# Optimization experiments

Measured on AMD Instinct MI355X. Metric: run time of the kernel, lower is better.

The kernel has to match this reference:

```python
import jax, jax.numpy as jnp
import numpy as np

D_IN = 1024
D_OUT = 1024
NUM_HEADS = 16
HEAD_DIM = D_OUT // NUM_HEADS


def setup_inputs() -> dict:
    key = jax.random.key(0)
    ks = jax.random.split(key, 6)
    scale = 0.02
    x = jax.random.normal(ks[0], (8, 1024, D_IN), dtype=jnp.float32)
    # weights stored as [in, out] (transposed vs torch Linear.weight)
    W_query = jax.random.normal(ks[1], (D_IN, D_OUT), dtype=jnp.float32) * scale
    W_key = jax.random.normal(ks[2], (D_IN, HEAD_DIM), dtype=jnp.float32) * scale
    W_value = jax.random.normal(ks[3], (D_IN, HEAD_DIM), dtype=jnp.float32) * scale
    W_out = jax.random.normal(ks[4], (D_OUT, D_OUT), dtype=jnp.float32) * scale
    b_out = jax.random.normal(ks[5], (D_OUT,), dtype=jnp.float32) * scale
    return {"x": x, "W_query": W_query, "W_key": W_key, "W_value": W_value,
            "W_out": W_out, "b_out": b_out}


def reference(x, W_query, W_key, W_value, W_out, b_out):
    B, S, _ = x.shape
    H, Dh = NUM_HEADS, HEAD_DIM
    q = (x @ W_query).reshape(B, S, H, Dh).transpose(0, 2, 1, 3)  # [B,H,S,Dh]
    k = x @ W_key      # [B,S,Dh] single shared head
    v = x @ W_value    # [B,S,Dh]
    # scores: broadcast shared K across all query heads (no explicit repeat)
    scores = jnp.einsum("bhqd,bkd->bhqk", q, k)  # [B,H,S,S]
    causal = jnp.triu(jnp.ones((S, S), dtype=bool), k=1)
    scores = jnp.where(causal[None, None], -jnp.inf, scores)
    attn = jax.nn.softmax(scores / np.sqrt(Dh).astype(np.float32), axis=-1)
    # dropout p=0.0 -> identity
    ctx = jnp.einsum("bhqk,bkd->bhqd", attn, v)  # [B,H,S,Dh]
    ctx = ctx.transpose(0, 2, 1, 3).reshape(B, S, H * Dh)
    return ctx @ W_out + b_out
```

## Files before the change

### kernel.cpp

```cpp
#include <hip/hip_runtime.h>

typedef unsigned short u16;
typedef __attribute__((ext_vector_type(8))) short short8;
typedef __attribute__((ext_vector_type(4))) float f32x4;
typedef __attribute__((ext_vector_type(16))) float f32x16;
typedef __attribute__((ext_vector_type(4))) unsigned short u16x4;
typedef __attribute__((ext_vector_type(4))) int i32x4;

__device__ __forceinline__ u16 f2b(float f) {
  unsigned u = __float_as_uint(f);
  unsigned r = (u + 0x7fffu + ((u >> 16) & 1u)) >> 16;
  return (u16)r;
}

__device__ __forceinline__ void gload16(const u16* g, u16* l) {
  __builtin_amdgcn_global_load_lds((const __attribute__((address_space(1))) void*)g,
                                   (__attribute__((address_space(3))) void*)l, 16, 0, 0);
}

__global__ void cvt_bf16(const float* __restrict__ in, u16* __restrict__ out, int n) {
  int i = (blockIdx.x * blockDim.x + threadIdx.x) * 4;
  if (i >= n) return;
  f32x4 v = *(const f32x4*)(in + i);
  u16x4 o;
  o[0] = f2b(v[0]); o[1] = f2b(v[1]); o[2] = f2b(v[2]); o[3] = f2b(v[3]);
  *(u16x4*)(out + i) = o;
}

__global__ void transpose_cvt(const float* __restrict__ in, u16* __restrict__ out, int R, int C) {
  __shared__ float t[32][33];
  int c0 = blockIdx.x * 32, r0 = blockIdx.y * 32;
  int tx = threadIdx.x & 31, ty = threadIdx.x >> 5;
#pragma unroll
  for (int i = 0; i < 32; i += 8)
    t[ty + i][tx] = in[(size_t)(r0 + ty + i) * C + c0 + tx];
  __syncthreads();
#pragma unroll
  for (int i = 0; i < 32; i += 8)
    out[(size_t)(c0 + ty + i) * R + r0 + tx] = f2b(t[tx][ty + i]);
}

#define GEMM_CORE(A_PTR, B_PTR)                                                        \
  __shared__ u16 As[4096];                                                \
  __shared__ u16 Bs[8192];                                               \
  const int tid = threadIdx.x;                                                         \
  const int lane = tid & 63, wid = tid >> 6;                              \
  const int lg = lane >> 4, li = lane & 15;                                            \
  const int wr = wid >> 1, wc = wid & 1;                                               \
  f32x4 acc[2][4] = {};                                                                \
  const int lrow = lane >> 3;                                                \
  const int lslot = lane & 7;                                                          \
  const int scol = 8 * (lslot ^ lrow);                    \
  const u16* Ab = (A_PTR) + (size_t)(m0 + wid * 16 + lrow) * 1024 + scol;              \
  const u16* Bb = (B_PTR) + (size_t)(wid * 32 + lrow) * 1024 + scol;                   \
  u16* const dA = As + wid * 1024;                   \
  u16* const dB = Bs + wid * 2048;                                                     \
  for (int t = 0; t < 16; ++t) {                                                       \
    const int k0 = t * 64;                                                             \
    __syncthreads();                                       \
    gload16(Ab + k0,         dA);                                                      \
    gload16(Ab + k0 + 8192,  dA + 512);                                   \
    _Pragma("unroll")                                                                  \
    for (int c = 0; c < 4; ++c)                                                        \
      gload16(Bb + k0 + c * 8192, dB + c * 512);                                       \
    __syncthreads();                                          \
    _Pragma("unroll")                                                                  \
    for (int kki = 0; kki < 2; ++kki) {                                                \
      short8 af[2], bfr[4];                                                            \
      _Pragma("unroll")                                                                \
      for (int mi = 0; mi < 2; ++mi) {                                                 \
        const int r = wr * 32 + mi * 16 + li;                                          \
        af[mi] = *(const short8*)&As[r * 64 + 8 * ((4 * kki + lg) ^ (r & 7))];         \
      }                                                                                \
      _Pragma("unroll")                                                                \
      for (int ni = 0; ni < 4; ++ni) {                                                 \
        const int r = wc * 64 + ni * 16 + li;                                          \
        bfr[ni] = *(const short8*)&Bs[r * 64 + 8 * ((4 * kki + lg) ^ (r & 7))];        \
      }                                                                                \
      _Pragma("unroll")                                                                \
      for (int mi = 0; mi < 2; ++mi)                                                   \
        _Pragma("unroll")                                                              \
        for (int ni = 0; ni < 4; ++ni)                                                 \
          acc[mi][ni] =                                                                \
              __builtin_amdgcn_mfma_f32_16x16x32_bf16(af[mi], bfr[ni], acc[mi][ni],    \
                                                      0, 0, 0);                        \
    }                                                                                  \
  }

__global__ __launch_bounds__(256) void gemm_proj(
    const u16* __restrict__ A, const u16* __restrict__ BtQ, const u16* __restrict__ BtKV,
    u16* __restrict__ Qp, u16* __restrict__ K3, u16* __restrict__ Vt3, float scaleQ) {
  const int m0 = blockIdx.x * 64;
  const int by = blockIdx.y;
  const bool isQ = (by < 8);
  const int n0 = isQ ? by * 128 : 0;
  GEMM_CORE(A, (isQ ? BtQ + (size_t)n0 * 1024 : BtKV))

#pragma unroll
  for (int mi = 0; mi < 2; ++mi) {
#pragma unroll
    for (int ni = 0; ni < 4; ++ni) {
      const int n = n0 + wc * 64 + ni * 16 + li;
#pragma unroll
      for (int i = 0; i < 4; ++i) {
        const int m = m0 + wr * 32 + mi * 16 + lg * 4 + i;
        const float v = acc[mi][ni][i];
        const int bb = m >> 10, ss = m & 1023;
        const int qt = ss >> 5, sl = ss & 31;
        if (isQ) {
          const int h = n >> 6, dd = n & 63;
          const int t = dd >> 4, h2 = (dd >> 3) & 1, j = dd & 7;
          Qp[(((((size_t)bb * 16 + h) * 32 + qt) * 4 + t) * 2 + h2) * 256 + sl * 8 + j] =
              f2b(v * scaleQ);
        } else if (n < 64) {
          const int t = n >> 4, h2 = (n >> 3) & 1, j = n & 7;
          K3[(((((size_t)bb * 32 + qt) * 4 + t) * 2 + h2) * 32 + sl) * 8 + j] = f2b(v);
        } else {
          const int d = n - 64;
          const int ks = sl >> 4, rem = sl & 15;
          const int h2 = (rem >> 2) & 1, j = (rem & 3) | ((rem >> 3) << 2);
          Vt3[(((((size_t)bb * 32 + qt) * 2 + ks) * 2 + h2) * 64 + d) * 8 + j] = f2b(v);
        }
      }
    }
  }
}

__global__ __launch_bounds__(256) void gemm_out(
    const u16* __restrict__ A, const u16* __restrict__ Bt,
    float* __restrict__ Cf, const float* __restrict__ bias) {
  const int m0 = blockIdx.x * 64;
  const int n0 = blockIdx.y * 128;
  GEMM_CORE(A, Bt + (size_t)n0 * 1024)

#pragma unroll
  for (int mi = 0; mi < 2; ++mi)
#pragma unroll
    for (int ni = 0; ni < 4; ++ni) {
      const int n = n0 + wc * 64 + ni * 16 + li;
#pragma unroll
      for (int i = 0; i < 4; ++i) {
        const int m = m0 + wr * 32 + mi * 16 + lg * 4 + i;
        Cf[(size_t)m * 1024 + n] = acc[mi][ni][i] + bias[n];
      }
    }
}

__global__ __launch_bounds__(256, 4) void attn_mqa6(
    const u16* __restrict__ qp, const u16* __restrict__ k3,
    const u16* __restrict__ vt3, u16* __restrict__ paro, float* __restrict__ pl) {
  __shared__ u16 lk[2][2048];
  __shared__ u16 lv[2][2048];
  const int lane = threadIdx.x & 63, wid = threadIdx.x >> 6;
  const int bx = blockIdx.x;
  const int qt = 31 - (bx >> 6);
  const int s  = (bx >> 5) & 1;
  const int g  = bx & 31;
  const int b  = g >> 2;
  const int h  = (g & 3) * 4 + wid;
  const int l31 = lane & 31, hi = lane >> 5;
  const int n0t = (qt + 2) >> 1;
  const int kb_ = s ? n0t : 0;
  const int ke  = s ? qt + 1 : n0t;
  const int task = (b * 16 + h) * 32 + qt;

  const u16* k3b = k3 + (size_t)b * 65536;
  const u16* v3b = vt3 + (size_t)b * 65536;
  const int soff = wid * 512 + lane * 8;

  const u16* qbase = qp + (size_t)task * 2048 + hi * 256 + l31 * 8;
  short8 qa[4];
#pragma unroll
  for (int t = 0; t < 4; ++t) qa[t] = *(const short8*)(qbase + t * 512);

  f32x16 acc0 = {}, acc1 = {};
  float lsum = 0.f;

  if (kb_ < ke) {
    gload16(k3b + (size_t)kb_ * 2048 + soff, &lk[0][wid * 512]);
    gload16(v3b + (size_t)kb_ * 2048 + soff, &lv[0][wid * 512]);
    __syncthreads();

    int par = 0;
    for (int kvt = kb_; kvt < ke; ++kvt, par ^= 1) {
      if (kvt + 1 < ke) {
        gload16(k3b + (size_t)(kvt + 1) * 2048 + soff, &lk[par ^ 1][wid * 512]);
        gload16(v3b + (size_t)(kvt + 1) * 2048 + soff, &lv[par ^ 1][wid * 512]);
      }
      short8 kc[4];
#pragma unroll
      for (int t = 0; t < 4; ++t)
        kc[t] = *(const short8*)&lk[par][l31 * 8 + (t * 2 + hi) * 256];
      const u16* vtt = &lv[par][hi * 512 + l31 * 8];
      const short8 vf0 = *(const short8*)(vtt);
      const short8 vf1 = *(const short8*)(vtt + 1024);
      const short8 vf2 = *(const short8*)(vtt + 256);
      const short8 vf3 = *(const short8*)(vtt + 1280);

      f32x16 st = {};
#pragma unroll
      for (int t = 0; t < 4; ++t)
        st = __builtin_amdgcn_mfma_f32_32x32x16_bf16(kc[t], qa[t], st, 0, 0, 0);

      if (kvt == qt) {
#pragma unroll
        for (int r = 0; r < 16; ++r) {
          const int crow = (r & 3) + 8 * (r >> 2) + 4 * hi;
          if (crow > l31) st[r] = -1e38f;
        }
      }
      float e[16];
#pragma unroll
      for (int r = 0; r < 16; ++r)
        asm("v_exp_f32 %0, %1" : "=v"(e[r]) : "v"(st[r]));
      lsum += ((e[0] + e[1]) + (e[2] + e[3])) + ((e[4] + e[5]) + (e[6] + e[7])) +
              (((e[8] + e[9]) + (e[10] + e[11])) + ((e[12] + e[13]) + (e[14] + e[15])));

      unsigned pw0, pw1, pw2, pw3, pw4, pw5, pw6, pw7;
      asm("v_cvt_pk_bf16_f32 %0, %1, %2" : "=v"(pw0) : "v"(e[0]),  "v"(e[1]));
      asm("v_cvt_pk_bf16_f32 %0, %1, %2" : "=v"(pw1) : "v"(e[2]),  "v"(e[3]));
      asm("v_cvt_pk_bf16_f32 %0, %1, %2" : "=v"(pw2) : "v"(e[4]),  "v"(e[5]));
      asm("v_cvt_pk_bf16_f32 %0, %1, %2" : "=v"(pw3) : "v"(e[6]),  "v"(e[7]));
      asm("v_cvt_pk_bf16_f32 %0, %1, %2" : "=v"(pw4) : "v"(e[8]),  "v"(e[9]));
      asm("v_cvt_pk_bf16_f32 %0, %1, %2" : "=v"(pw5) : "v"(e[10]), "v"(e[11]));
      asm("v_cvt_pk_bf16_f32 %0, %1, %2" : "=v"(pw6) : "v"(e[12]), "v"(e[13]));
      asm("v_cvt_pk_bf16_f32 %0, %1, %2" : "=v"(pw7) : "v"(e[14]), "v"(e[15]));
      i32x4 w0 = {(int)pw0, (int)pw1, (int)pw2, (int)pw3};
      i32x4 w1 = {(int)pw4, (int)pw5, (int)pw6, (int)pw7};
      const short8 pa0 = *(const short8*)&w0;
      const short8 pa1 = *(const short8*)&w1;

      acc0 = __builtin_amdgcn_mfma_f32_32x32x16_bf16(pa0, vf0, acc0, 0, 0, 0);
      acc0 = __builtin_amdgcn_mfma_f32_32x32x16_bf16(pa1, vf1, acc0, 0, 0, 0);
      acc1 = __builtin_amdgcn_mfma_f32_32x32x16_bf16(pa0, vf2, acc1, 0, 0, 0);
      acc1 = __builtin_amdgcn_mfma_f32_32x32x16_bf16(pa1, vf3, acc1, 0, 0, 0);

      __syncthreads();
    }
  }

  const float lfull = lsum + __shfl_xor(lsum, 32, 64);
  u16* pbase = paro + ((size_t)task * 2 + s) * 2048;
#pragma unroll
  for (int r = 0; r < 16; ++r) {
    const int crow = (r & 3) + 8 * (r >> 2) + 4 * hi;
    pbase[crow * 64 + l31] = f2b(acc0[r]);
    pbase[crow * 64 + 32 + l31] = f2b(acc1[r]);
  }
  if (hi == 0) pl[((size_t)task * 2 + s) * 32 + l31] = lfull;
}

__global__ __launch_bounds__(256) void attn_combine(
    const u16* __restrict__ paro, const float* __restrict__ pl, u16* __restrict__ ctxb) {
  const int grp = threadIdx.x >> 6, tid = threadIdx.x & 63;
  const int task = blockIdx.x * 4 + grp;
  const int qt = task & 31, hh = (task >> 5) & 15, bb = task >> 9;
  const unsigned* p0 = (const unsigned*)(paro + (size_t)task * 4096);
  const unsigned* p1 = p0 + 1024;
  const float* lt = pl + (size_t)task * 64;
  const int rh = tid >> 5, cc = tid & 31;
  unsigned* co = (unsigned*)ctxb;
#pragma unroll 4
  for (int it = 0; it < 16; ++it) {
    const int r = it * 2 + rh;
    const float inv = 1.0f / (lt[r] + lt[32 + r]);
    const unsigned a = p0[r * 32 + cc], bu = p1[r * 32 + cc];
    const float v0 = (__uint_as_float(a << 16) + __uint_as_float(bu << 16)) * inv;
    const float v1 = (__uint_as_float(a & 0xffff0000u) + __uint_as_float(bu & 0xffff0000u)) * inv;
    const unsigned pk = (unsigned)f2b(v0) | ((unsigned)f2b(v1) << 16);
    co[(size_t)(bb * 1024 + qt * 32 + r) * 512 + hh * 32 + cc] = pk;
  }
}

extern "C" void kernel_launch(void* const* d_in, const int* in_sizes, int n_in,
                              void* d_out, int out_size, void* d_ws, size_t ws_size,
                              hipStream_t stream) {
  const float* x  = (const float*)d_in[0];
  const float* Wq = (const float*)d_in[1];
  const float* Wk = (const float*)d_in[2];
  const float* Wv = (const float*)d_in[3];
  const float* Wo = (const float*)d_in[4];
  const float* bo = (const float*)d_in[5];
  float* out = (float*)d_out;

  u16* ws16 = (u16*)d_ws;
  const size_t M1 = 1u << 20;
  u16* woT  = ws16;
  u16* qp   = ws16 + 1 * M1;
  u16* k3   = ws16 + 9 * M1;
  u16* vt3  = ws16 + 9 * M1 + (M1 >> 1);
  u16* xb   = ws16 + 10 * M1;
  u16* wqT  = ws16 + 18 * M1;
  u16* wkT  = ws16 + 19 * M1;
  u16* wvT  = wkT + 65536;
  u16* paro = ws16 + 10 * M1;
  float* pl = (float*)(ws16 + 26 * M1);
  u16* ctx  = qp;

  cvt_bf16<<<8192, 256, 0, stream>>>(x, xb, 8192 * 1024);
  transpose_cvt<<<dim3(32, 32), 256, 0, stream>>>(Wq, wqT, 1024, 1024);
  transpose_cvt<<<dim3(2, 32), 256, 0, stream>>>(Wk, wkT, 1024, 64);
  transpose_cvt<<<dim3(2, 32), 256, 0, stream>>>(Wv, wvT, 1024, 64);
  transpose_cvt<<<dim3(32, 32), 256, 0, stream>>>(Wo, woT, 1024, 1024);

  const float SCL = 0.125f * 1.44269504088896340736f;
  gemm_proj<<<dim3(128, 9), 256, 0, stream>>>(xb, wqT, wkT, qp, k3, vt3, SCL);

  attn_mqa6<<<2048, 256, 0, stream>>>(qp, k3, vt3, paro, pl);
  attn_combine<<<1024, 256, 0, stream>>>(paro, pl, ctx);

  gemm_out<<<dim3(128, 8), 256, 0, stream>>>(ctx, woT, out, bo);
}
```

Baseline: 115.4 us.

## Double-buffer GEMM LDS tiles and drop split-KV attention with combine kernel

The shared GEMM core now double-buffers its A and B tiles in LDS, issuing the next k-tile's global-to-LDS loads before computing on the current tile, so load latency overlaps MFMA work. The attention kernel no longer splits each query tile's KV range into two halves. It uses 128-thread blocks, two heads per block, each covering the full causal KV range, and normalises and writes bf16 context directly. This removes the separate combine kernel and its partial-output round trip through memory. The cost is double the LDS in the GEMMs and less parallelism, with more load imbalance across causal tiles in attention.

```diff
diff --git a/kernel.cpp b/kernel.cpp
--- a/kernel.cpp
+++ b/kernel.cpp
@@ -41,41 +41,49 @@
 }
 
 #define GEMM_CORE(A_PTR, B_PTR)                                                        \
-  __shared__ u16 As[4096];                                                \
-  __shared__ u16 Bs[8192];                                               \
+  __shared__ u16 As[2][4096];                                             \
+  __shared__ u16 Bs[2][8192];                                            \
   const int tid = threadIdx.x;                                                         \
   const int lane = tid & 63, wid = tid >> 6;                              \
   const int lg = lane >> 4, li = lane & 15;                                            \
   const int wr = wid >> 1, wc = wid & 1;                                               \
   f32x4 acc[2][4] = {};                                                                \
-  const int lrow = lane >> 3;                                                \
-  const int lslot = lane & 7;                                                          \
+  const int lrow = lane >> 3, lslot = lane & 7;                                        \
   const int scol = 8 * (lslot ^ lrow);                    \
   const u16* Ab = (A_PTR) + (size_t)(m0 + wid * 16 + lrow) * 1024 + scol;              \
   const u16* Bb = (B_PTR) + (size_t)(wid * 32 + lrow) * 1024 + scol;                   \
-  u16* const dA = As + wid * 1024;                   \
-  u16* const dB = Bs + wid * 2048;                                                     \
-  for (int t = 0; t < 16; ++t) {                                                       \
-    const int k0 = t * 64;                                                             \
-    __syncthreads();                                       \
-    gload16(Ab + k0,         dA);                                                      \
-    gload16(Ab + k0 + 8192,  dA + 512);                                   \
-    _Pragma("unroll")                                                                  \
-    for (int c = 0; c < 4; ++c)                                                        \
-      gload16(Bb + k0 + c * 8192, dB + c * 512);                                       \
-    __syncthreads();                                          \
+  const int dAo = wid * 1024, dBo = wid * 2048;            \
+  gload16(Ab, &As[0][dAo]);                                                            \
+  gload16(Ab + 8192, &As[0][dAo + 512]);                                               \
+  { _Pragma("unroll")                                                                  \
+    for (int c_ = 0; c_ < 4; ++c_) gload16(Bb + c_ * 8192, &Bs[0][dBo + c_ * 512]); }  \
+  asm volatile("s_waitcnt vmcnt(0)" ::: "memory");                                     \
+  __builtin_amdgcn_s_barrier();                                                        \
+  __builtin_amdgcn_sched_barrier(0);                                                   \
+  int par = 0;                                                                         \
+  for (int t = 0; t < 16; ++t, par ^= 1) {                                             \
+    if (t < 15) {                                           \
+      const int k1 = (t + 1) * 64;                                                     \
+      gload16(Ab + k1, &As[par ^ 1][dAo]);                                             \
+      gload16(Ab + k1 + 8192, &As[par ^ 1][dAo + 512]);                                \
+      _Pragma("unroll")                                                                \
+      for (int c_ = 0; c_ < 4; ++c_)                                                   \
+        gload16(Bb + k1 + c_ * 8192, &Bs[par ^ 1][dBo + c_ * 512]);                    \
+    }                                                                                  \
+    const u16* Ac = As[par];                                                           \
+    const u16* Bc = Bs[par];                                                           \
     _Pragma("unroll")                                                                  \
     for (int kki = 0; kki < 2; ++kki) {                                                \
       short8 af[2], bfr[4];                                                            \
       _Pragma("unroll")                                                                \
       for (int mi = 0; mi < 2; ++mi) {                                                 \
         const int r = wr * 32 + mi * 16 + li;                                          \
-        af[mi] = *(const short8*)&As[r * 64 + 8 * ((4 * kki + lg) ^ (r & 7))];         \
+        af[mi] = *(const short8*)&Ac[r * 64 + 8 * ((4 * kki + lg) ^ (r & 7))];         \
       }                                                                                \
       _Pragma("unroll")                                                                \
       for (int ni = 0; ni < 4; ++ni) {                                                 \
         const int r = wc * 64 + ni * 16 + li;                                          \
-        bfr[ni] = *(const short8*)&Bs[r * 64 + 8 * ((4 * kki + lg) ^ (r & 7))];        \
+        bfr[ni] = *(const short8*)&Bc[r * 64 + 8 * ((4 * kki + lg) ^ (r & 7))];        \
       }                                                                                \
       _Pragma("unroll")                                                                \
       for (int mi = 0; mi < 2; ++mi)                                                   \
@@ -85,6 +93,9 @@
               __builtin_amdgcn_mfma_f32_16x16x32_bf16(af[mi], bfr[ni], acc[mi][ni],    \
                                                       0, 0, 0);                        \
     }                                                                                  \
+    asm volatile("s_waitcnt vmcnt(0)" ::: "memory");  \
+    __builtin_amdgcn_s_barrier();                     \
+    __builtin_amdgcn_sched_barrier(0);                                                 \
   }
 
 __global__ __launch_bounds__(256) void gemm_proj(
@@ -146,27 +157,26 @@
     }
 }
 
-__global__ __launch_bounds__(256, 4) void attn_mqa6(
+__global__ __launch_bounds__(128, 4) void attn_mqa7(
     const u16* __restrict__ qp, const u16* __restrict__ k3,
-    const u16* __restrict__ vt3, u16* __restrict__ paro, float* __restrict__ pl) {
+    const u16* __restrict__ vt3, u16* __restrict__ ctxb) {
   __shared__ u16 lk[2][2048];
   __shared__ u16 lv[2][2048];
   const int lane = threadIdx.x & 63, wid = threadIdx.x >> 6;
   const int bx = blockIdx.x;
   const int qt = 31 - (bx >> 6);
-  const int s  = (bx >> 5) & 1;
-  const int g  = bx & 31;
-  const int b  = g >> 2;
-  const int h  = (g & 3) * 4 + wid;
+  const int r6 = bx & 63;
+  const int b  = r6 >> 3;
+  const int h  = (r6 & 7) * 2 + wid;
   const int l31 = lane & 31, hi = lane >> 5;
-  const int n0t = (qt + 2) >> 1;
-  const int kb_ = s ? n0t : 0;
-  const int ke  = s ? qt + 1 : n0t;
+  const int q0 = qt * 32;
+  const int ke = qt + 1;
   const int task = (b * 16 + h) * 32 + qt;
 
   const u16* k3b = k3 + (size_t)b * 65536;
   const u16* v3b = vt3 + (size_t)b * 65536;
-  const int soff = wid * 512 + lane * 8;
+  const int soff = wid * 1024 + lane * 8;
+  const int dstw = wid * 1024;
 
   const u16* qbase = qp + (size_t)task * 2048 + hi * 256 + l31 * 8;
   short8 qa[4];
@@ -176,99 +186,81 @@
   f32x16 acc0 = {}, acc1 = {};
   float lsum = 0.f;
 
-  if (kb_ < ke) {
-    gload16(k3b + (size_t)kb_ * 2048 + soff, &lk[0][wid * 512]);
-    gload16(v3b + (size_t)kb_ * 2048 + soff, &lv[0][wid * 512]);
+  gload16(k3b + soff,       &lk[0][dstw]);
+  gload16(k3b + soff + 512, &lk[0][dstw + 512]);
+  gload16(v3b + soff,       &lv[0][dstw]);
+  gload16(v3b + soff + 512, &lv[0][dstw + 512]);
+  __syncthreads();
+
+  int par = 0;
+  for (int kvt = 0; kvt < ke; ++kvt, par ^= 1) {
+    if (kvt + 1 < ke) {
+      const size_t o = (size_t)(kvt + 1) * 2048 + soff;
+      gload16(k3b + o,       &lk[par ^ 1][dstw]);
+      gload16(k3b + o + 512, &lk[par ^ 1][dstw + 512]);
+      gload16(v3b + o,       &lv[par ^ 1][dstw]);
+      gload16(v3b + o + 512, &lv[par ^ 1][dstw + 512]);
+    }
+    short8 kc[4];
+#pragma unroll
+    for (int t = 0; t < 4; ++t)
+      kc[t] = *(const short8*)&lk[par][l31 * 8 + (t * 2 + hi) * 256];
+    const u16* vtt = &lv[par][hi * 512 + l31 * 8];
+    const short8 vf0 = *(const short8*)(vtt);
+    const short8 vf1 = *(const short8*)(vtt + 1024);
+    const short8 vf2 = *(const short8*)(vtt + 256);
+    const short8 vf3 = *(const short8*)(vtt + 1280);
+
+    f32x16 st = {};
+#pragma unroll
+    for (int t = 0; t < 4; ++t)
+      st = __builtin_amdgcn_mfma_f32_32x32x16_bf16(kc[t], qa[t], st, 0, 0, 0);
+
+    if (kvt == qt) {
+#pragma unroll
+      for (int r = 0; r < 16; ++r) {
+        const int crow = (r & 3) + 8 * (r >> 2) + 4 * hi;
+        if (crow > l31) st[r] = -1e38f;
+      }
+    }
+    float e[16];
+#pragma unroll
+    for (int r = 0; r < 16; ++r)
+      asm("v_exp_f32 %0, %1" : "=v"(e[r]) : "v"(st[r]));
+    lsum += ((e[0] + e[1]) + (e[2] + e[3])) + ((e[4] + e[5]) + (e[6] + e[7])) +
+            (((e[8] + e[9]) + (e[10] + e[11])) + ((e[12] + e[13]) + (e[14] + e[15])));
+
+    unsigned pw0, pw1, pw2, pw3, pw4, pw5, pw6, pw7;
+    asm("v_cvt_pk_bf16_f32 %0, %1, %2" : "=v"(pw0) : "v"(e[0]),  "v"(e[1]));
+    asm("v_cvt_pk_bf16_f32 %0, %1, %2" : "=v"(pw1) : "v"(e[2]),  "v"(e[3]));
+    asm("v_cvt_pk_bf16_f32 %0, %1, %2" : "=v"(pw2) : "v"(e[4]),  "v"(e[5]));
+    asm("v_cvt_pk_bf16_f32 %0, %1, %2" : "=v"(pw3) : "v"(e[6]),  "v"(e[7]));
+    asm("v_cvt_pk_bf16_f32 %0, %1, %2" : "=v"(pw4) : "v"(e[8]),  "v"(e[9]));
+    asm("v_cvt_pk_bf16_f32 %0, %1, %2" : "=v"(pw5) : "v"(e[10]), "v"(e[11]));
+    asm("v_cvt_pk_bf16_f32 %0, %1, %2" : "=v"(pw6) : "v"(e[12]), "v"(e[13]));
+    asm("v_cvt_pk_bf16_f32 %0, %1, %2" : "=v"(pw7) : "v"(e[14]), "v"(e[15]));
+    i32x4 w0 = {(int)pw0, (int)pw1, (int)pw2, (int)pw3};
+    i32x4 w1 = {(int)pw4, (int)pw5, (int)pw6, (int)pw7};
+    const short8 pa0 = *(const short8*)&w0;
+    const short8 pa1 = *(const short8*)&w1;
+
+    acc0 = __builtin_amdgcn_mfma_f32_32x32x16_bf16(pa0, vf0, acc0, 0, 0, 0);
+    acc0 = __builtin_amdgcn_mfma_f32_32x32x16_bf16(pa1, vf1, acc0, 0, 0, 0);
+    acc1 = __builtin_amdgcn_mfma_f32_32x32x16_bf16(pa0, vf2, acc1, 0, 0, 0);
+    acc1 = __builtin_amdgcn_mfma_f32_32x32x16_bf16(pa1, vf3, acc1, 0, 0, 0);
+
     __syncthreads();
-
-    int par = 0;
-    for (int kvt = kb_; kvt < ke; ++kvt, par ^= 1) {
-      if (kvt + 1 < ke) {
-        gload16(k3b + (size_t)(kvt + 1) * 2048 + soff, &lk[par ^ 1][wid * 512]);
-        gload16(v3b + (size_t)(kvt + 1) * 2048 + soff, &lv[par ^ 1][wid * 512]);
-      }
-      short8 kc[4];
-#pragma unroll
-      for (int t = 0; t < 4; ++t)
-        kc[t] = *(const short8*)&lk[par][l31 * 8 + (t * 2 + hi) * 256];
-      const u16* vtt = &lv[par][hi * 512 + l31 * 8];
-      const short8 vf0 = *(const short8*)(vtt);
-      const short8 vf1 = *(const short8*)(vtt + 1024);
-      const short8 vf2 = *(const short8*)(vtt + 256);
-      const short8 vf3 = *(const short8*)(vtt + 1280);
-
-      f32x16 st = {};
-#pragma unroll
-      for (int t = 0; t < 4; ++t)
-        st = __builtin_amdgcn_mfma_f32_32x32x16_bf16(kc[t], qa[t], st, 0, 0, 0);
-
-      if (kvt == qt) {
-#pragma unroll
-        for (int r = 0; r < 16; ++r) {
-          const int crow = (r & 3) + 8 * (r >> 2) + 4 * hi;
-          if (crow > l31) st[r] = -1e38f;
-        }
-      }
-      float e[16];
-#pragma unroll
-      for (int r = 0; r < 16; ++r)
-        asm("v_exp_f32 %0, %1" : "=v"(e[r]) : "v"(st[r]));
-      lsum += ((e[0] + e[1]) + (e[2] + e[3])) + ((e[4] + e[5]) + (e[6] + e[7])) +
-              (((e[8] + e[9]) + (e[10] + e[11])) + ((e[12] + e[13]) + (e[14] + e[15])));
-
-      unsigned pw0, pw1, pw2, pw3, pw4, pw5, pw6, pw7;
-      asm("v_cvt_pk_bf16_f32 %0, %1, %2" : "=v"(pw0) : "v"(e[0]),  "v"(e[1]));
-      asm("v_cvt_pk_bf16_f32 %0, %1, %2" : "=v"(pw1) : "v"(e[2]),  "v"(e[3]));
-      asm("v_cvt_pk_bf16_f32 %0, %1, %2" : "=v"(pw2) : "v"(e[4]),  "v"(e[5]));
-      asm("v_cvt_pk_bf16_f32 %0, %1, %2" : "=v"(pw3) : "v"(e[6]),  "v"(e[7]));
-      asm("v_cvt_pk_bf16_f32 %0, %1, %2" : "=v"(pw4) : "v"(e[8]),  "v"(e[9]));
-      asm("v_cvt_pk_bf16_f32 %0, %1, %2" : "=v"(pw5) : "v"(e[10]), "v"(e[11]));
-      asm("v_cvt_pk_bf16_f32 %0, %1, %2" : "=v"(pw6) : "v"(e[12]), "v"(e[13]));
-      asm("v_cvt_pk_bf16_f32 %0, %1, %2" : "=v"(pw7) : "v"(e[14]), "v"(e[15]));
-      i32x4 w0 = {(int)pw0, (int)pw1, (int)pw2, (int)pw3};
-      i32x4 w1 = {(int)pw4, (int)pw5, (int)pw6, (int)pw7};
-      const short8 pa0 = *(const short8*)&w0;
-      const short8 pa1 = *(const short8*)&w1;
-
-      acc0 = __builtin_amdgcn_mfma_f32_32x32x16_bf16(pa0, vf0, acc0, 0, 0, 0);
-      acc0 = __builtin_amdgcn_mfma_f32_32x32x16_bf16(pa1, vf1, acc0, 0, 0, 0);
-      acc1 = __builtin_amdgcn_mfma_f32_32x32x16_bf16(pa0, vf2, acc1, 0, 0, 0);
-      acc1 = __builtin_amdgcn_mfma_f32_32x32x16_bf16(pa1, vf3, acc1, 0, 0, 0);
-
-      __syncthreads();
-    }
   }
 
   const float lfull = lsum + __shfl_xor(lsum, 32, 64);
-  u16* pbase = paro + ((size_t)task * 2 + s) * 2048;
+  const float linv = 1.0f / lfull;
 #pragma unroll
   for (int r = 0; r < 16; ++r) {
     const int crow = (r & 3) + 8 * (r >> 2) + 4 * hi;
-    pbase[crow * 64 + l31] = f2b(acc0[r]);
-    pbase[crow * 64 + 32 + l31] = f2b(acc1[r]);
-  }
-  if (hi == 0) pl[((size_t)task * 2 + s) * 32 + l31] = lfull;
-}
-
-__global__ __launch_bounds__(256) void attn_combine(
-    const u16* __restrict__ paro, const float* __restrict__ pl, u16* __restrict__ ctxb) {
-  const int grp = threadIdx.x >> 6, tid = threadIdx.x & 63;
-  const int task = blockIdx.x * 4 + grp;
-  const int qt = task & 31, hh = (task >> 5) & 15, bb = task >> 9;
-  const unsigned* p0 = (const unsigned*)(paro + (size_t)task * 4096);
-  const unsigned* p1 = p0 + 1024;
-  const float* lt = pl + (size_t)task * 64;
-  const int rh = tid >> 5, cc = tid & 31;
-  unsigned* co = (unsigned*)ctxb;
-#pragma unroll 4
-  for (int it = 0; it < 16; ++it) {
-    const int r = it * 2 + rh;
-    const float inv = 1.0f / (lt[r] + lt[32 + r]);
-    const unsigned a = p0[r * 32 + cc], bu = p1[r * 32 + cc];
-    const float v0 = (__uint_as_float(a << 16) + __uint_as_float(bu << 16)) * inv;
-    const float v1 = (__uint_as_float(a & 0xffff0000u) + __uint_as_float(bu & 0xffff0000u)) * inv;
-    const unsigned pk = (unsigned)f2b(v0) | ((unsigned)f2b(v1) << 16);
-    co[(size_t)(bb * 1024 + qt * 32 + r) * 512 + hh * 32 + cc] = pk;
+    const float lr = __shfl(linv, crow, 64);
+    const size_t mrow = (size_t)(b * 1024 + q0 + crow) * 1024 + h * 64;
+    ctxb[mrow + l31] = f2b(acc0[r] * lr);
+    ctxb[mrow + 32 + l31] = f2b(acc1[r] * lr);
   }
 }
 
@@ -290,12 +282,10 @@
   u16* k3   = ws16 + 9 * M1;
   u16* vt3  = ws16 + 9 * M1 + (M1 >> 1);
   u16* xb   = ws16 + 10 * M1;
+  u16* ctx  = ws16 + 10 * M1;
   u16* wqT  = ws16 + 18 * M1;
   u16* wkT  = ws16 + 19 * M1;
   u16* wvT  = wkT + 65536;
-  u16* paro = ws16 + 10 * M1;
-  float* pl = (float*)(ws16 + 26 * M1);
-  u16* ctx  = qp;
 
   cvt_bf16<<<8192, 256, 0, stream>>>(x, xb, 8192 * 1024);
   transpose_cvt<<<dim3(32, 32), 256, 0, stream>>>(Wq, wqT, 1024, 1024);
@@ -306,8 +296,7 @@
   const float SCL = 0.125f * 1.44269504088896340736f;
   gemm_proj<<<dim3(128, 9), 256, 0, stream>>>(xb, wqT, wkT, qp, k3, vt3, SCL);
 
-  attn_mqa6<<<2048, 256, 0, stream>>>(qp, k3, vt3, paro, pl);
-  attn_combine<<<1024, 256, 0, stream>>>(paro, pl, ctx);
+  attn_mqa7<<<2048, 128, 0, stream>>>(qp, k3, vt3, ctx);
 
   gemm_out<<<dim3(128, 8), 256, 0, stream>>>(ctx, woT, out, bo);
 }
```

New measurement: 125.3 us. 8.6% more time.

## Fuse prep conversion kernels and triple-buffer the output GEMM loads

Applied to the files above, without the earlier changes.

Merges the x bf16 conversion and the four weight transpose-convert launches into a single prep kernel that dispatches on block index, removing four kernel launches. It also adds a triple-buffered GEMM core for the output projection: it prefetches two k-tiles ahead with global_load_lds, waits on vmcnt and uses one barrier per iteration instead of two. This is meant to overlap global loads with MFMA work. The cost is three times the LDS per block, which may reduce occupancy, and the hand-written waitcnt assumes a fixed count of outstanding loads.

```diff
diff --git a/kernel.cpp b/kernel.cpp
--- a/kernel.cpp
+++ b/kernel.cpp
@@ -18,19 +18,30 @@
                                    (__attribute__((address_space(3))) void*)l, 16, 0, 0);
 }
 
-__global__ void cvt_bf16(const float* __restrict__ in, u16* __restrict__ out, int n) {
-  int i = (blockIdx.x * blockDim.x + threadIdx.x) * 4;
-  if (i >= n) return;
-  f32x4 v = *(const f32x4*)(in + i);
-  u16x4 o;
-  o[0] = f2b(v[0]); o[1] = f2b(v[1]); o[2] = f2b(v[2]); o[3] = f2b(v[3]);
-  *(u16x4*)(out + i) = o;
-}
-
-__global__ void transpose_cvt(const float* __restrict__ in, u16* __restrict__ out, int R, int C) {
+__global__ void prep(const float* __restrict__ x, const float* __restrict__ Wq,
+                     const float* __restrict__ Wk, const float* __restrict__ Wv,
+                     const float* __restrict__ Wo, u16* __restrict__ xb,
+                     u16* __restrict__ wqT, u16* __restrict__ wkT,
+                     u16* __restrict__ wvT, u16* __restrict__ woT) {
   __shared__ float t[32][33];
-  int c0 = blockIdx.x * 32, r0 = blockIdx.y * 32;
-  int tx = threadIdx.x & 31, ty = threadIdx.x >> 5;
+  int bid = blockIdx.x;
+  if (bid < 8192) {
+    const int i = (bid * 256 + threadIdx.x) * 4;
+    f32x4 v = *(const f32x4*)(x + i);
+    u16x4 o;
+    o[0] = f2b(v[0]); o[1] = f2b(v[1]); o[2] = f2b(v[2]); o[3] = f2b(v[3]);
+    *(u16x4*)(xb + i) = o;
+    return;
+  }
+  bid -= 8192;
+  const float* in; u16* out; int C, bx, by;
+  if (bid < 1024)      { in = Wq; out = wqT; C = 1024; bx = bid & 31; by = bid >> 5; }
+  else if (bid < 1088) { in = Wk; out = wkT; C = 64;   bid -= 1024; bx = bid & 1; by = bid >> 1; }
+  else if (bid < 1152) { in = Wv; out = wvT; C = 64;   bid -= 1088; bx = bid & 1; by = bid >> 1; }
+  else                 { in = Wo; out = woT; C = 1024; bid -= 1152; bx = bid & 31; by = bid >> 5; }
+  const int R = 1024;
+  const int c0 = bx * 32, r0 = by * 32;
+  const int tx = threadIdx.x & 31, ty = threadIdx.x >> 5;
 #pragma unroll
   for (int i = 0; i < 32; i += 8)
     t[ty + i][tx] = in[(size_t)(r0 + ty + i) * C + c0 + tx];
@@ -48,22 +59,20 @@
   const int lg = lane >> 4, li = lane & 15;                                            \
   const int wr = wid >> 1, wc = wid & 1;                                               \
   f32x4 acc[2][4] = {};                                                                \
-  const int lrow = lane >> 3;                                                \
-  const int lslot = lane & 7;                                                          \
+  const int lrow = lane >> 3, lslot = lane & 7;                                        \
   const int scol = 8 * (lslot ^ lrow);                    \
   const u16* Ab = (A_PTR) + (size_t)(m0 + wid * 16 + lrow) * 1024 + scol;              \
   const u16* Bb = (B_PTR) + (size_t)(wid * 32 + lrow) * 1024 + scol;                   \
-  u16* const dA = As + wid * 1024;                   \
+  u16* const dA = As + wid * 1024;                                                     \
   u16* const dB = Bs + wid * 2048;                                                     \
   for (int t = 0; t < 16; ++t) {                                                       \
     const int k0 = t * 64;                                                             \
-    __syncthreads();                                       \
-    gload16(Ab + k0,         dA);                                                      \
-    gload16(Ab + k0 + 8192,  dA + 512);                                   \
+    __syncthreads();                                                                   \
+    gload16(Ab + k0,        dA);                                                       \
+    gload16(Ab + k0 + 8192, dA + 512);                                                 \
     _Pragma("unroll")                                                                  \
-    for (int c = 0; c < 4; ++c)                                                        \
-      gload16(Bb + k0 + c * 8192, dB + c * 512);                                       \
-    __syncthreads();                                          \
+    for (int c_ = 0; c_ < 4; ++c_) gload16(Bb + k0 + c_ * 8192, dB + c_ * 512);        \
+    __syncthreads();                                                                   \
     _Pragma("unroll")                                                                  \
     for (int kki = 0; kki < 2; ++kki) {                                                \
       short8 af[2], bfr[4];                                                            \
@@ -85,6 +94,67 @@
               __builtin_amdgcn_mfma_f32_16x16x32_bf16(af[mi], bfr[ni], acc[mi][ni],    \
                                                       0, 0, 0);                        \
     }                                                                                  \
+  }
+
+#define GEMM_CORE_DEEP(A_PTR, B_PTR)                                                   \
+  __shared__ u16 As[3][4096];                                                          \
+  __shared__ u16 Bs[3][8192];                                                          \
+  const int tid = threadIdx.x;                                                         \
+  const int lane = tid & 63, wid = tid >> 6;                                           \
+  const int lg = lane >> 4, li = lane & 15;                                            \
+  const int wr = wid >> 1, wc = wid & 1;                                               \
+  f32x4 acc[2][4] = {};                                                                \
+  const int lrow = lane >> 3, lslot = lane & 7;                                        \
+  const int scol = 8 * (lslot ^ lrow);                                                 \
+  const u16* Ab = (A_PTR) + (size_t)(m0 + wid * 16 + lrow) * 1024 + scol;              \
+  const u16* Bb = (B_PTR) + (size_t)(wid * 32 + lrow) * 1024 + scol;                   \
+  const int dAo = wid * 1024, dBo = wid * 2048;                                        \
+  _Pragma("unroll")                                                                    \
+  for (int p = 0; p < 2; ++p) {                                                        \
+    const int kp = p * 64;                                                             \
+    gload16(Ab + kp,        &As[p][dAo]);                                              \
+    gload16(Ab + kp + 8192, &As[p][dAo + 512]);                                        \
+    _Pragma("unroll")                                                                  \
+    for (int c_ = 0; c_ < 4; ++c_) gload16(Bb + kp + c_ * 8192, &Bs[p][dBo + c_ * 512]); \
+  }                                                                                    \
+  int cur = 0;                                                                         \
+  for (int t = 0; t < 16; ++t) {                                                       \
+    if (t < 15) asm volatile("s_waitcnt vmcnt(6)" ::: "memory");                       \
+    else        asm volatile("s_waitcnt vmcnt(0)" ::: "memory");                       \
+    __builtin_amdgcn_s_barrier();                                                      \
+    __builtin_amdgcn_sched_barrier(0);                                                 \
+    if (t + 2 < 16) {                                                                  \
+      const int k2 = (t + 2) * 64;                                                     \
+      const int nb = (cur + 2 >= 3) ? cur - 1 : cur + 2;                               \
+      gload16(Ab + k2,        &As[nb][dAo]);                                           \
+      gload16(Ab + k2 + 8192, &As[nb][dAo + 512]);                                     \
+      _Pragma("unroll")                                                                \
+      for (int c_ = 0; c_ < 4; ++c_) gload16(Bb + k2 + c_ * 8192, &Bs[nb][dBo + c_ * 512]); \
+    }                                                                                  \
+    const u16* Ac = As[cur];                                                           \
+    const u16* Bc = Bs[cur];                                                           \
+    _Pragma("unroll")                                                                  \
+    for (int kki = 0; kki < 2; ++kki) {                                                \
+      short8 af[2], bfr[4];                                                            \
+      _Pragma("unroll")                                                                \
+      for (int mi = 0; mi < 2; ++mi) {                                                 \
+        const int r = wr * 32 + mi * 16 + li;                                          \
+        af[mi] = *(const short8*)&Ac[r * 64 + 8 * ((4 * kki + lg) ^ (r & 7))];         \
+      }                                                                                \
+      _Pragma("unroll")                                                                \
+      for (int ni = 0; ni < 4; ++ni) {                                                 \
+        const int r = wc * 64 + ni * 16 + li;                                          \
+        bfr[ni] = *(const short8*)&Bc[r * 64 + 8 * ((4 * kki + lg) ^ (r & 7))];        \
+      }                                                                                \
+      _Pragma("unroll")                                                                \
+      for (int mi = 0; mi < 2; ++mi)                                                   \
+        _Pragma("unroll")                                                              \
+        for (int ni = 0; ni < 4; ++ni)                                                 \
+          acc[mi][ni] =                                                                \
+              __builtin_amdgcn_mfma_f32_16x16x32_bf16(af[mi], bfr[ni], acc[mi][ni],    \
+                                                      0, 0, 0);                        \
+    }                                                                                  \
+    cur = (cur == 2) ? 0 : cur + 1;                                                    \
   }
 
 __global__ __launch_bounds__(256) void gemm_proj(
@@ -131,7 +201,7 @@
     float* __restrict__ Cf, const float* __restrict__ bias) {
   const int m0 = blockIdx.x * 64;
   const int n0 = blockIdx.y * 128;
-  GEMM_CORE(A, Bt + (size_t)n0 * 1024)
+  GEMM_CORE_DEEP(A, Bt + (size_t)n0 * 1024)
 
 #pragma unroll
   for (int mi = 0; mi < 2; ++mi)
@@ -297,11 +367,7 @@
   float* pl = (float*)(ws16 + 26 * M1);
   u16* ctx  = qp;
 
-  cvt_bf16<<<8192, 256, 0, stream>>>(x, xb, 8192 * 1024);
-  transpose_cvt<<<dim3(32, 32), 256, 0, stream>>>(Wq, wqT, 1024, 1024);
-  transpose_cvt<<<dim3(2, 32), 256, 0, stream>>>(Wk, wkT, 1024, 64);
-  transpose_cvt<<<dim3(2, 32), 256, 0, stream>>>(Wv, wvT, 1024, 64);
-  transpose_cvt<<<dim3(32, 32), 256, 0, stream>>>(Wo, woT, 1024, 1024);
+  prep<<<10368, 256, 0, stream>>>(x, Wq, Wk, Wv, Wo, xb, wqT, wkT, wvT, woT);
 
   const float SCL = 0.125f * 1.44269504088896340736f;
   gemm_proj<<<dim3(128, 9), 256, 0, stream>>>(xb, wqT, wkT, qp, k3, vt3, SCL);
```

Measured after the change: 115.4 us. About the same (+0.1%).

## Fuse split-KV attention combine into attention kernel and merge prep kernels

Applied to the files above, without the earlier changes.

Restructures the attention kernel so each block runs two heads, each split across two waves over KV ranges. The two halves are merged in-block through shared memory, normalised and written directly as bf16 context. This removes the separate combine kernel and the partial-output and row-sum round trip through global memory. The five conversion and transpose launches are also folded into one prep kernel, cutting launch overhead. In exchange, the causal split leaves waves idle on unequal KV ranges, blocks now load different K/V tiles per wave pair, and there is an extra block-wide sync for the merge.

```diff
diff --git a/kernel.cpp b/kernel.cpp
--- a/kernel.cpp
+++ b/kernel.cpp
@@ -18,19 +18,30 @@
                                    (__attribute__((address_space(3))) void*)l, 16, 0, 0);
 }
 
-__global__ void cvt_bf16(const float* __restrict__ in, u16* __restrict__ out, int n) {
-  int i = (blockIdx.x * blockDim.x + threadIdx.x) * 4;
-  if (i >= n) return;
-  f32x4 v = *(const f32x4*)(in + i);
-  u16x4 o;
-  o[0] = f2b(v[0]); o[1] = f2b(v[1]); o[2] = f2b(v[2]); o[3] = f2b(v[3]);
-  *(u16x4*)(out + i) = o;
-}
-
-__global__ void transpose_cvt(const float* __restrict__ in, u16* __restrict__ out, int R, int C) {
+__global__ void prep(const float* __restrict__ x, const float* __restrict__ Wq,
+                     const float* __restrict__ Wk, const float* __restrict__ Wv,
+                     const float* __restrict__ Wo, u16* __restrict__ xb,
+                     u16* __restrict__ wqT, u16* __restrict__ wkT,
+                     u16* __restrict__ wvT, u16* __restrict__ woT) {
   __shared__ float t[32][33];
-  int c0 = blockIdx.x * 32, r0 = blockIdx.y * 32;
-  int tx = threadIdx.x & 31, ty = threadIdx.x >> 5;
+  int bid = blockIdx.x;
+  if (bid < 8192) {
+    const int i = (bid * 256 + threadIdx.x) * 4;
+    f32x4 v = *(const f32x4*)(x + i);
+    u16x4 o;
+    o[0] = f2b(v[0]); o[1] = f2b(v[1]); o[2] = f2b(v[2]); o[3] = f2b(v[3]);
+    *(u16x4*)(xb + i) = o;
+    return;
+  }
+  bid -= 8192;
+  const float* in; u16* out; int C, bx, by;
+  if (bid < 1024)      { in = Wq; out = wqT; C = 1024; bx = bid & 31; by = bid >> 5; }
+  else if (bid < 1088) { in = Wk; out = wkT; C = 64;   bid -= 1024; bx = bid & 1; by = bid >> 1; }
+  else if (bid < 1152) { in = Wv; out = wvT; C = 64;   bid -= 1088; bx = bid & 1; by = bid >> 1; }
+  else                 { in = Wo; out = woT; C = 1024; bid -= 1152; bx = bid & 31; by = bid >> 5; }
+  const int R = 1024;
+  const int c0 = bx * 32, r0 = by * 32;
+  const int tx = threadIdx.x & 31, ty = threadIdx.x >> 5;
 #pragma unroll
   for (int i = 0; i < 32; i += 8)
     t[ty + i][tx] = in[(size_t)(r0 + ty + i) * C + c0 + tx];
@@ -48,22 +59,20 @@
   const int lg = lane >> 4, li = lane & 15;                                            \
   const int wr = wid >> 1, wc = wid & 1;                                               \
   f32x4 acc[2][4] = {};                                                                \
-  const int lrow = lane >> 3;                                                \
-  const int lslot = lane & 7;                                                          \
+  const int lrow = lane >> 3, lslot = lane & 7;                                        \
   const int scol = 8 * (lslot ^ lrow);                    \
   const u16* Ab = (A_PTR) + (size_t)(m0 + wid * 16 + lrow) * 1024 + scol;              \
   const u16* Bb = (B_PTR) + (size_t)(wid * 32 + lrow) * 1024 + scol;                   \
-  u16* const dA = As + wid * 1024;                   \
+  u16* const dA = As + wid * 1024;                                                     \
   u16* const dB = Bs + wid * 2048;                                                     \
   for (int t = 0; t < 16; ++t) {                                                       \
     const int k0 = t * 64;                                                             \
-    __syncthreads();                                       \
-    gload16(Ab + k0,         dA);                                                      \
-    gload16(Ab + k0 + 8192,  dA + 512);                                   \
+    __syncthreads();                                                                   \
+    gload16(Ab + k0,        dA);                                                       \
+    gload16(Ab + k0 + 8192, dA + 512);                                                 \
     _Pragma("unroll")                                                                  \
-    for (int c = 0; c < 4; ++c)                                                        \
-      gload16(Bb + k0 + c * 8192, dB + c * 512);                                       \
-    __syncthreads();                                          \
+    for (int c_ = 0; c_ < 4; ++c_) gload16(Bb + k0 + c_ * 8192, dB + c_ * 512);        \
+    __syncthreads();                                                                   \
     _Pragma("unroll")                                                                  \
     for (int kki = 0; kki < 2; ++kki) {                                                \
       short8 af[2], bfr[4];                                                            \
@@ -146,27 +155,30 @@
     }
 }
 
-__global__ __launch_bounds__(256, 4) void attn_mqa6(
+__global__ __launch_bounds__(256, 4) void attn_mqa8(
     const u16* __restrict__ qp, const u16* __restrict__ k3,
-    const u16* __restrict__ vt3, u16* __restrict__ paro, float* __restrict__ pl) {
-  __shared__ u16 lk[2][2048];
-  __shared__ u16 lv[2][2048];
+    const u16* __restrict__ vt3, u16* __restrict__ ctxb) {
+  __shared__ __align__(16) u16 smem[16384];
   const int lane = threadIdx.x & 63, wid = threadIdx.x >> 6;
   const int bx = blockIdx.x;
   const int qt = 31 - (bx >> 6);
-  const int s  = (bx >> 5) & 1;
-  const int g  = bx & 31;
-  const int b  = g >> 2;
-  const int h  = (g & 3) * 4 + wid;
+  const int r6 = bx & 63;
+  const int b  = r6 >> 3;
+  const int hp = r6 & 7;
+  const int hh = wid & 1;
+  const int s  = wid >> 1;
+  const int h  = hp * 2 + hh;
   const int l31 = lane & 31, hi = lane >> 5;
   const int n0t = (qt + 2) >> 1;
-  const int kb_ = s ? n0t : 0;
-  const int ke  = s ? qt + 1 : n0t;
+  const int cs  = s ? (qt + 1 - n0t) : n0t;
+  const int base = s ? n0t : 0;
   const int task = (b * 16 + h) * 32 + qt;
 
   const u16* k3b = k3 + (size_t)b * 65536;
   const u16* v3b = vt3 + (size_t)b * 65536;
-  const int soff = wid * 512 + lane * 8;
+  const int sreg = s * 4096;
+  const int doff = hh * 1024;
+  const int loff = lane * 8;
 
   const u16* qbase = qp + (size_t)task * 2048 + hi * 256 + l31 * 8;
   short8 qa[4];
@@ -176,22 +188,34 @@
   f32x16 acc0 = {}, acc1 = {};
   float lsum = 0.f;
 
-  if (kb_ < ke) {
-    gload16(k3b + (size_t)kb_ * 2048 + soff, &lk[0][wid * 512]);
-    gload16(v3b + (size_t)kb_ * 2048 + soff, &lv[0][wid * 512]);
-    __syncthreads();
-
-    int par = 0;
-    for (int kvt = kb_; kvt < ke; ++kvt, par ^= 1) {
-      if (kvt + 1 < ke) {
-        gload16(k3b + (size_t)(kvt + 1) * 2048 + soff, &lk[par ^ 1][wid * 512]);
-        gload16(v3b + (size_t)(kvt + 1) * 2048 + soff, &lv[par ^ 1][wid * 512]);
-      }
+  if (cs > 0) {
+    const size_t o = (size_t)base * 2048 + doff + loff;
+    gload16(k3b + o,       &smem[sreg + doff]);
+    gload16(k3b + o + 512, &smem[sreg + doff + 512]);
+    gload16(v3b + o,       &smem[8192 + sreg + doff]);
+    gload16(v3b + o + 512, &smem[8192 + sreg + doff + 512]);
+  }
+  __syncthreads();
+
+  int par = 0;
+  for (int i = 0; i < n0t; ++i, par ^= 1) {
+    if (i + 1 < cs) {
+      const size_t o = (size_t)(base + i + 1) * 2048 + doff + loff;
+      const int dst = sreg + (par ^ 1) * 2048 + doff;
+      gload16(k3b + o,       &smem[dst]);
+      gload16(k3b + o + 512, &smem[dst + 512]);
+      gload16(v3b + o,       &smem[8192 + dst]);
+      gload16(v3b + o + 512, &smem[8192 + dst + 512]);
+    }
+    if (i < cs) {
+      const int kvt = base + i;
+      const u16* lkb = &smem[sreg + par * 2048];
+      const u16* lvb = &smem[8192 + sreg + par * 2048];
       short8 kc[4];
 #pragma unroll
       for (int t = 0; t < 4; ++t)
-        kc[t] = *(const short8*)&lk[par][l31 * 8 + (t * 2 + hi) * 256];
-      const u16* vtt = &lv[par][hi * 512 + l31 * 8];
+        kc[t] = *(const short8*)&lkb[l31 * 8 + (t * 2 + hi) * 256];
+      const u16* vtt = &lvb[hi * 512 + l31 * 8];
       const short8 vf0 = *(const short8*)(vtt);
       const short8 vf1 = *(const short8*)(vtt + 1024);
       const short8 vf2 = *(const short8*)(vtt + 256);
@@ -234,41 +258,36 @@
       acc0 = __builtin_amdgcn_mfma_f32_32x32x16_bf16(pa1, vf1, acc0, 0, 0, 0);
       acc1 = __builtin_amdgcn_mfma_f32_32x32x16_bf16(pa0, vf2, acc1, 0, 0, 0);
       acc1 = __builtin_amdgcn_mfma_f32_32x32x16_bf16(pa1, vf3, acc1, 0, 0, 0);
-
-      __syncthreads();
-    }
+    }
+    __syncthreads();
   }
 
   const float lfull = lsum + __shfl_xor(lsum, 32, 64);
-  u16* pbase = paro + ((size_t)task * 2 + s) * 2048;
-#pragma unroll
-  for (int r = 0; r < 16; ++r) {
-    const int crow = (r & 3) + 8 * (r >> 2) + 4 * hi;
-    pbase[crow * 64 + l31] = f2b(acc0[r]);
-    pbase[crow * 64 + 32 + l31] = f2b(acc1[r]);
-  }
-  if (hi == 0) pl[((size_t)task * 2 + s) * 32 + l31] = lfull;
-}
-
-__global__ __launch_bounds__(256) void attn_combine(
-    const u16* __restrict__ paro, const float* __restrict__ pl, u16* __restrict__ ctxb) {
-  const int grp = threadIdx.x >> 6, tid = threadIdx.x & 63;
-  const int task = blockIdx.x * 4 + grp;
-  const int qt = task & 31, hh = (task >> 5) & 15, bb = task >> 9;
-  const unsigned* p0 = (const unsigned*)(paro + (size_t)task * 4096);
-  const unsigned* p1 = p0 + 1024;
-  const float* lt = pl + (size_t)task * 64;
-  const int rh = tid >> 5, cc = tid & 31;
-  unsigned* co = (unsigned*)ctxb;
-#pragma unroll 4
-  for (int it = 0; it < 16; ++it) {
-    const int r = it * 2 + rh;
-    const float inv = 1.0f / (lt[r] + lt[32 + r]);
-    const unsigned a = p0[r * 32 + cc], bu = p1[r * 32 + cc];
-    const float v0 = (__uint_as_float(a << 16) + __uint_as_float(bu << 16)) * inv;
-    const float v1 = (__uint_as_float(a & 0xffff0000u) + __uint_as_float(bu & 0xffff0000u)) * inv;
-    const unsigned pk = (unsigned)f2b(v0) | ((unsigned)f2b(v1) << 16);
-    co[(size_t)(bb * 1024 + qt * 32 + r) * 512 + hh * 32 + cc] = pk;
+  float* exf = (float*)smem;
+  if (s == 1) {
+    float* ab = exf + hh * 2048 + lane * 32;
+#pragma unroll
+    for (int r = 0; r < 16; ++r) {
+      ab[(2 * r) ^ (lane & 31)] = acc0[r];
+      ab[(2 * r + 1) ^ (lane & 31)] = acc1[r];
+    }
+    exf[4096 + hh * 64 + lane] = lfull;
+  }
+  __syncthreads();
+  if (s == 0) {
+    const float lfp = exf[4096 + hh * 64 + lane];
+    const float linv = 1.0f / (lfull + lfp);
+    const float* ab = exf + hh * 2048 + lane * 32;
+#pragma unroll
+    for (int r = 0; r < 16; ++r) {
+      const int crow = (r & 3) + 8 * (r >> 2) + 4 * hi;
+      const float lr = __shfl(linv, crow, 64);
+      const float o0 = acc0[r] + ab[(2 * r) ^ (lane & 31)];
+      const float o1 = acc1[r] + ab[(2 * r + 1) ^ (lane & 31)];
+      const size_t mrow = (size_t)(b * 1024 + qt * 32 + crow) * 1024 + h * 64;
+      ctxb[mrow + l31] = f2b(o0 * lr);
+      ctxb[mrow + 32 + l31] = f2b(o1 * lr);
+    }
   }
 }
 
@@ -290,24 +309,17 @@
   u16* k3   = ws16 + 9 * M1;
   u16* vt3  = ws16 + 9 * M1 + (M1 >> 1);
   u16* xb   = ws16 + 10 * M1;
+  u16* ctx  = ws16 + 10 * M1;
   u16* wqT  = ws16 + 18 * M1;
   u16* wkT  = ws16 + 19 * M1;
   u16* wvT  = wkT + 65536;
-  u16* paro = ws16 + 10 * M1;
-  float* pl = (float*)(ws16 + 26 * M1);
-  u16* ctx  = qp;
-
-  cvt_bf16<<<8192, 256, 0, stream>>>(x, xb, 8192 * 1024);
-  transpose_cvt<<<dim3(32, 32), 256, 0, stream>>>(Wq, wqT, 1024, 1024);
-  transpose_cvt<<<dim3(2, 32), 256, 0, stream>>>(Wk, wkT, 1024, 64);
-  transpose_cvt<<<dim3(2, 32), 256, 0, stream>>>(Wv, wvT, 1024, 64);
-  transpose_cvt<<<dim3(32, 32), 256, 0, stream>>>(Wo, woT, 1024, 1024);
+
+  prep<<<10368, 256, 0, stream>>>(x, Wq, Wk, Wv, Wo, xb, wqT, wkT, wvT, woT);
 
   const float SCL = 0.125f * 1.44269504088896340736f;
   gemm_proj<<<dim3(128, 9), 256, 0, stream>>>(xb, wqT, wkT, qp, k3, vt3, SCL);
 
-  attn_mqa6<<<2048, 256, 0, stream>>>(qp, k3, vt3, paro, pl);
-  attn_combine<<<1024, 256, 0, stream>>>(paro, pl, ctx);
+  attn_mqa8<<<2048, 256, 0, stream>>>(qp, k3, vt3, ctx);
 
   gemm_out<<<dim3(128, 8), 256, 0, stream>>>(ctx, woT, out, bo);
 }
```

Result: faster. 100.6 us (-12.8%).
